# Kernel optimization log

Hardware: AMD Instinct MI355X
Metric: run time of the kernel (lower is better)

The kernel has to match this reference:

```python
import jax, jax.numpy as jnp
import numpy as np

B, S, HID, H = 4, 2048, 768, 12
HD = HID // H  # head dim = 64
EPS = 1e-12


def _linear(x, w, b):
    # x: [B,S,HID], w: [HID,OUT] (already transposed to in x out), b: [OUT]
    return jnp.einsum('bsi,io->bso', x, w) + b


def _heads(x):
    # [B,S,HID] -> [B,H,S,HD]
    return x.reshape(B, S, H, HD).transpose(0, 2, 1, 3)


def _layernorm(x, g, b):
    mu = jnp.mean(x, axis=-1, keepdims=True)
    var = jnp.mean(jnp.square(x - mu), axis=-1, keepdims=True)
    return (x - mu) * jax.lax.rsqrt(var + EPS) * g + b


def _attend(q, k, v, mask):
    # q:[B,H,Sq,HD] k,v:[B,H,Sk,HD] mask:[B,1,1,Sk] additive
    scores = jnp.einsum('bhqd,bhkd->bhqk', q, k) / np.float32(np.sqrt(HD)) + mask
    probs = jax.nn.softmax(scores, axis=-1)  # dropout is identity in eval
    ctx = jnp.einsum('bhqk,bhkd->bhqd', probs, v)
    return ctx.transpose(0, 2, 1, 3).reshape(B, S, HID)


def setup_inputs() -> dict:
    key = jax.random.key(0)
    ks = jax.random.split(key, 20)
    std = 0.02
    mkw = lambda k: (jax.random.normal(k, (HID, HID), jnp.float32) * std)
    inp = {
        'input_tensor1': jax.random.normal(ks[0], (B, S, HID), jnp.float32),
        'attention_mask1': jnp.zeros((B, 1, 1, S), jnp.float32),
        'input_tensor2': jax.random.normal(ks[1], (B, S, HID), jnp.float32),
        'attention_mask2': jnp.zeros((B, 1, 1, S), jnp.float32),
        'q1_w': mkw(ks[2]), 'q1_b': jnp.zeros(HID),
        'k1_w': mkw(ks[3]), 'k1_b': jnp.zeros(HID),
        'v1_w': mkw(ks[4]), 'v1_b': jnp.zeros(HID),
        'q2_w': mkw(ks[5]), 'q2_b': jnp.zeros(HID),
        'k2_w': mkw(ks[6]), 'k2_b': jnp.zeros(HID),
        'v2_w': mkw(ks[7]), 'v2_b': jnp.zeros(HID),
        'd1_w': mkw(ks[8]), 'd1_b': jnp.zeros(HID),
        'd2_w': mkw(ks[9]), 'd2_b': jnp.zeros(HID),
        'ln1_g': jnp.ones(HID), 'ln1_b': jnp.zeros(HID),
        'ln2_g': jnp.ones(HID), 'ln2_b': jnp.zeros(HID),
    }
    return inp


def reference(input_tensor1, attention_mask1, input_tensor2, attention_mask2,
              q1_w, q1_b, k1_w, k1_b, v1_w, v1_b,
              q2_w, q2_b, k2_w, k2_b, v2_w, v2_b,
              d1_w, d1_b, d2_w, d2_b, ln1_g, ln1_b, ln2_g, ln2_b):
    q1 = _heads(_linear(input_tensor1, q1_w, q1_b))
    k1 = _heads(_linear(input_tensor1, k1_w, k1_b))
    v1 = _heads(_linear(input_tensor1, v1_w, v1_b))
    q2 = _heads(_linear(input_tensor2, q2_w, q2_b))
    k2 = _heads(_linear(input_tensor2, k2_w, k2_b))
    v2 = _heads(_linear(input_tensor2, v2_w, v2_b))
    # stream1 context: queries from stream2 attend keys/values of stream1
    ctx1 = _attend(q2, k1, v1, attention_mask1)
    # stream2 context: queries from stream1 attend keys/values of stream2
    ctx2 = _attend(q1, k2, v2, attention_mask2)
    h1 = _layernorm(_linear(ctx1, d1_w, d1_b) + input_tensor1, ln1_g, ln1_b)
    h2 = _layernorm(_linear(ctx2, d2_w, d2_b) + input_tensor2, ln2_g, ln2_b)
    return (h1, h2)
```

## Files before the change

### kernel.cpp

```cpp
#include <hip/hip_runtime.h>
#include <hip/hip_bf16.h>

#define BB   4
#define SS   2048
#define HID_ 768
#define NH   12
#define HD_  64
#define MR   8192
#define XELEMS 6291456

typedef __attribute__((ext_vector_type(8))) short short8;
typedef __attribute__((ext_vector_type(4))) float floatx4;

__device__ __forceinline__ unsigned short f2bf(float f) {
  union { float f; unsigned int u; } x; x.f = f;
  unsigned int r = x.u + 0x7fffu + ((x.u >> 16) & 1u);
  return (unsigned short)(r >> 16);
}

__device__ __forceinline__ unsigned int cvt_pk_bf16(float lo, float hi) {
  unsigned int r;
  asm("v_cvt_pk_bf16_f32 %0, %1, %2" : "=v"(r) : "v"(lo), "v"(hi));
  return r;
}

__device__ __forceinline__ void gload_lds16(const unsigned short* g, unsigned short* l) {
  __builtin_amdgcn_global_load_lds(
      (const __attribute__((address_space(1))) unsigned int*)g,
      (__attribute__((address_space(3))) unsigned int*)l, 16, 0, 0);
}

struct CastArgs { const float* src[2]; unsigned short* dst[2]; };

__global__ __launch_bounds__(256)
void cast_kernel(CastArgs a) {
  const int z = blockIdx.y;
  int i = (blockIdx.x * 256 + threadIdx.x) * 4;
  float4 v = *(const float4*)(a.src[z] + i);
  ushort4 o;
  o.x = f2bf(v.x); o.y = f2bf(v.y); o.z = f2bf(v.z); o.w = f2bf(v.w);
  *(ushort4*)(a.dst[z] + i) = o;
}

struct WArgs { const float* src[8]; unsigned short* dst[8]; };

__global__ __launch_bounds__(256)
void wcast_kernel(WArgs args) {
  __shared__ float tile[32][33];
  const int w = blockIdx.z;
  const float* __restrict__ src = args.src[w];
  unsigned short* __restrict__ dst = args.dst[w];
  const int n0 = blockIdx.x * 32, k0 = blockIdx.y * 32;
  const int tx = threadIdx.x & 31, ty = threadIdx.x >> 5;
  #pragma unroll
  for (int i = 0; i < 4; ++i)
    tile[ty + 8 * i][tx] = src[(size_t)(k0 + ty + 8 * i) * HID_ + n0 + tx];
  __syncthreads();
  #pragma unroll
  for (int i = 0; i < 4; ++i)
    dst[(size_t)(n0 + ty + 8 * i) * HID_ + k0 + tx] = f2bf(tile[tx][ty + 8 * i]);
}

struct GemmArgs {
  const unsigned short* A[6];
  const unsigned short* Bt[6];
  const float* bias[6];
  const float* resid[6];
  unsigned short* outb[6];
  float* outf[6];
  int tmode[6];
};

template <int MODE>
__global__ __launch_bounds__(256)
void gemm_kernel(GemmArgs args) {
  const int z = blockIdx.z;
  const unsigned short* __restrict__ A  = args.A[z];
  const unsigned short* __restrict__ Bt = args.Bt[z];
  const int m0 = blockIdx.x * 128;
  const int n0 = blockIdx.y * 128;

  __shared__ __align__(16) unsigned short a_sh[128 * 32];
  __shared__ __align__(16) unsigned short b_sh[128 * 32];

  const int tid  = threadIdx.x;
  const int lane = tid & 63;
  const int wave = tid >> 6;
  const int wm = (wave & 1) * 64;
  const int wn = (wave >> 1) * 64;
  const int l15 = lane & 15;
  const int ko  = lane >> 4;

  floatx4 acc[4][4];
  #pragma unroll
  for (int mt = 0; mt < 4; ++mt)
    #pragma unroll
    for (int nt = 0; nt < 4; ++nt) {
      floatx4 zz = {0.f, 0.f, 0.f, 0.f};
      acc[mt][nt] = zz;
    }

  const int ch0 = wave * 2;
  size_t aoff[2], boff[2];
  unsigned short *adst[2], *bdst[2];
  #pragma unroll
  for (int j = 0; j < 2; ++j) {
    const int ch = ch0 + j;
    const int row = ch * 16 + (lane >> 2);
    const int col = (lane & 3) * 8;
    aoff[j] = (size_t)(m0 + row) * 768 + col;
    boff[j] = (size_t)(n0 + row) * 768 + col;
    adst[j] = a_sh + ch * 512 + lane * 8;
    bdst[j] = b_sh + ch * 512 + lane * 8;
  }

  for (int k0 = 0; k0 < 768; k0 += 32) {
    #pragma unroll
    for (int j = 0; j < 2; ++j) {
      gload_lds16(A  + aoff[j] + k0, adst[j]);
      gload_lds16(Bt + boff[j] + k0, bdst[j]);
    }
    __syncthreads();
    short8 af[4], bfr[4];
    #pragma unroll
    for (int t = 0; t < 4; ++t) {
      af[t]  = *(const short8*)(a_sh + (wm + t * 16 + l15) * 32 + ko * 8);
      bfr[t] = *(const short8*)(b_sh + (wn + t * 16 + l15) * 32 + ko * 8);
    }
    #pragma unroll
    for (int mt = 0; mt < 4; ++mt)
      #pragma unroll
      for (int nt = 0; nt < 4; ++nt)
        acc[mt][nt] = __builtin_amdgcn_mfma_f32_16x16x32_bf16(af[mt], bfr[nt], acc[mt][nt], 0, 0, 0);
    __syncthreads();
  }

  if (MODE == 0) {
    const float* __restrict__ bias = args.bias[z];
    unsigned short* __restrict__ out = args.outb[z];
    if (args.tmode[z] == 0) {
      #pragma unroll
      for (int mt = 0; mt < 4; ++mt) {
        const int gm = m0 + wm + mt * 16 + ko * 4;
        #pragma unroll
        for (int nt = 0; nt < 4; ++nt) {
          const int gn = n0 + wn + nt * 16 + l15;
          const float bv = bias[gn];
          #pragma unroll
          for (int r = 0; r < 4; ++r)
            out[(size_t)(gm + r) * 768 + gn] = f2bf(acc[mt][nt][r] + bv);
        }
      }
    } else {
      #pragma unroll
      for (int mt = 0; mt < 4; ++mt) {
        const int gm = m0 + wm + mt * 16 + ko * 4;
        const int bb_ = gm >> 11;
        const int s   = gm & 2047;
        #pragma unroll
        for (int nt = 0; nt < 4; ++nt) {
          const int gn = n0 + wn + nt * 16 + l15;
          const float bv = bias[gn];
          const int h = gn >> 6, d = gn & 63;
          ushort4 o4;
          o4.x = f2bf(acc[mt][nt][0] + bv);
          o4.y = f2bf(acc[mt][nt][1] + bv);
          o4.z = f2bf(acc[mt][nt][2] + bv);
          o4.w = f2bf(acc[mt][nt][3] + bv);
          *(ushort4*)(out + ((size_t)((bb_ * 12 + h) * 64 + d)) * 2048 + s) = o4;
        }
      }
    }
  } else {
    const float* __restrict__ bias  = args.bias[z];
    const float* __restrict__ resid = args.resid[z];
    float* __restrict__ out = args.outf[z];
    #pragma unroll
    for (int mt = 0; mt < 4; ++mt) {
      const int gm = m0 + wm + mt * 16 + ko * 4;
      #pragma unroll
      for (int nt = 0; nt < 4; ++nt) {
        const int gn = n0 + wn + nt * 16 + l15;
        const float bv = bias[gn];
        #pragma unroll
        for (int r = 0; r < 4; ++r)
          out[(size_t)(gm + r) * 768 + gn] = acc[mt][nt][r] + bv + resid[(size_t)(gm + r) * 768 + gn];
      }
    }
  }
}

struct AttnArgs {
  const unsigned short* q[2];
  const unsigned short* k[2];
  const unsigned short* vt[2];
  const float* mask[2];
  unsigned short* ctx[2];
};

__global__ __launch_bounds__(256, 2)
void attn_kernel(AttnArgs args) {
  const int z = blockIdx.z;
  const int b = z >> 1, w = z & 1;
  const int h = blockIdx.y;
  const int q0 = blockIdx.x * 256;

  const unsigned short* __restrict__ Q  = args.q[1 - w];
  const unsigned short* __restrict__ K  = args.k[w];
  const unsigned short* __restrict__ Vt = args.vt[w] + ((size_t)(b * 12 + h)) * 64 * 2048;
  const float* __restrict__ mask = args.mask[w] + (size_t)b * SS;
  unsigned short* __restrict__ O = args.ctx[w];

  __shared__ __align__(16) unsigned short kv_sh[2][8192];
  __shared__ __align__(16) unsigned short p_sh[4][64 * 40];

  const int tid  = threadIdx.x;
  const int lane = tid & 63;
  const int wave = tid >> 6;
  const int l15 = lane & 15;
  const int lq  = lane >> 4;
  const int sw8 = (lq ^ (l15 & 3)) * 8;

  const unsigned short* gbase;
  int gadv;
  int goff[4];
  {
    const int rl = lane >> 2;
    const int jb = (lane & 3) ^ (rl & 3);
    if (wave < 2) {
      gbase = K + (size_t)(b * SS) * 768 + h * 64 + (wave & 1) * 32;
      gadv  = 64 * 768;
      #pragma unroll
      for (int j = 0; j < 4; ++j) goff[j] = (j * 16 + rl) * 768 + jb * 8;
    } else {
      gbase = Vt + (wave & 1) * 32;
      gadv  = 64;
      #pragma unroll
      for (int j = 0; j < 4; ++j) goff[j] = (j * 16 + rl) * 2048 + jb * 8;
    }
  }

  short8 qf[4][2];
  #pragma unroll
  for (int mt = 0; mt < 4; ++mt) {
    const size_t qrow = (size_t)(b * SS + q0 + wave * 64 + mt * 16 + l15) * 768 + h * 64;
    qf[mt][0] = *(const short8*)(Q + qrow + lq * 8);
    qf[mt][1] = *(const short8*)(Q + qrow + 32 + lq * 8);
  }

  floatx4 oacc[4][4];
  #pragma unroll
  for (int mt = 0; mt < 4; ++mt)
    #pragma unroll
    for (int nt = 0; nt < 4; ++nt) { floatx4 zz = {0.f,0.f,0.f,0.f}; oacc[mt][nt] = zz; }
  float lad[4];
  #pragma unroll
  for (int mt = 0; mt < 4; ++mt) lad[mt] = 0.f;

  const float SCL2 = 0.125f * 1.4426950408889634f;
  const float L2E  = 1.4426950408889634f;

  float4 mk_cur[4], mk_nxt[4];
  #pragma unroll
  for (int nt = 0; nt < 4; ++nt) mk_cur[nt] = *(const float4*)(mask + nt * 16 + lq * 4);
  #pragma unroll
  for (int j = 0; j < 4; ++j)
    gload_lds16(gbase + goff[j], &kv_sh[0][0] + (wave * 4 + j) * 512);
  gbase += gadv;

  unsigned short* const pw = p_sh[wave];
  const int NT = SS / 64;

  for (int t = 0; t < NT; ++t) {
    const int cb = t & 1;
    if (t + 1 < NT) {
      const int kt1 = (t + 1) * 64;
      #pragma unroll
      for (int nt = 0; nt < 4; ++nt)
        mk_nxt[nt] = *(const float4*)(mask + kt1 + nt * 16 + lq * 4);
      #pragma unroll
      for (int j = 0; j < 4; ++j)
        gload_lds16(gbase + goff[j], &kv_sh[cb ^ 1][0] + (wave * 4 + j) * 512);
      gbase += gadv;
      asm volatile("s_waitcnt vmcnt(8)" ::: "memory");
    } else {
      asm volatile("s_waitcnt vmcnt(0)" ::: "memory");
    }
    __builtin_amdgcn_s_barrier();
    asm volatile("" ::: "memory");

    const unsigned short* kb = &kv_sh[cb][0];
    const unsigned short* vb = &kv_sh[cb][4096];

    #pragma unroll
    for (int ksh = 0; ksh < 2; ++ksh) {
      #pragma unroll
      for (int ntk = 0; ntk < 2; ++ntk) {
        const int nt = ksh * 2 + ntk;
        const int ro = (nt * 16 + l15) * 32 + sw8;
        const short8 kf0 = *(const short8*)(kb + ro);
        const short8 kf1 = *(const short8*)(kb + 2048 + ro);
        const float m0 = mk_cur[nt].x * L2E;
        const float m1 = mk_cur[nt].y * L2E;
        const float m2 = mk_cur[nt].z * L2E;
        const float m3 = mk_cur[nt].w * L2E;
        #pragma unroll
        for (int mt = 0; mt < 4; ++mt) {
          floatx4 zz = {0.f,0.f,0.f,0.f};
          floatx4 sacc = __builtin_amdgcn_mfma_f32_16x16x32_bf16(kf0, qf[mt][0], zz, 0, 0, 0);
          sacc = __builtin_amdgcn_mfma_f32_16x16x32_bf16(kf1, qf[mt][1], sacc, 0, 0, 0);
          const float p0 = __builtin_amdgcn_exp2f(sacc[0] * SCL2 + m0);
          const float p1 = __builtin_amdgcn_exp2f(sacc[1] * SCL2 + m1);
          const float p2 = __builtin_amdgcn_exp2f(sacc[2] * SCL2 + m2);
          const float p3 = __builtin_amdgcn_exp2f(sacc[3] * SCL2 + m3);
          lad[mt] += (p0 + p1) + (p2 + p3);
          uint2 pk2;
          pk2.x = cvt_pk_bf16(p0, p1);
          pk2.y = cvt_pk_bf16(p2, p3);
          *(uint2*)(pw + (mt * 16 + l15) * 40 + ntk * 16 + lq * 4) = pk2;
        }
      }
      short8 vf[4];
      #pragma unroll
      for (int ntd = 0; ntd < 4; ++ntd)
        vf[ntd] = *(const short8*)(vb + ksh * 2048 + (ntd * 16 + l15) * 32 + sw8);
      #pragma unroll
      for (int mt = 0; mt < 4; ++mt) {
        const short8 pf = *(const short8*)(pw + (mt * 16 + l15) * 40 + lq * 8);
        #pragma unroll
        for (int ntd = 0; ntd < 4; ++ntd)
          oacc[mt][ntd] = __builtin_amdgcn_mfma_f32_16x16x32_bf16(pf, vf[ntd], oacc[mt][ntd], 0, 0, 0);
      }
    }

    asm volatile("" ::: "memory");
    __builtin_amdgcn_s_barrier();
    asm volatile("" ::: "memory");

    #pragma unroll
    for (int nt = 0; nt < 4; ++nt) mk_cur[nt] = mk_nxt[nt];
  }

  #pragma unroll
  for (int mt = 0; mt < 4; ++mt) {
    float ls = lad[mt];
    ls += __shfl_xor(ls, 16);
    ls += __shfl_xor(ls, 32);
    const float linv = 1.f / ls;
    float inv[4];
    #pragma unroll
    for (int r = 0; r < 4; ++r) inv[r] = __shfl(linv, lq * 4 + r, 16);
    #pragma unroll
    for (int nt = 0; nt < 4; ++nt) {
      #pragma unroll
      for (int r = 0; r < 4; ++r) {
        const int gq = q0 + wave * 64 + mt * 16 + lq * 4 + r;
        const int gd = h * 64 + nt * 16 + l15;
        O[(size_t)(b * SS + gq) * 768 + gd] = f2bf(oacc[mt][nt][r] * inv[r]);
      }
    }
  }
}

struct LnArgs { const float* src[2]; const float* g[2]; const float* bta[2]; float* out[2]; };

__global__ __launch_bounds__(256)
void ln_kernel(LnArgs a) {
  const int z = blockIdx.y;
  const int row = blockIdx.x;
  const int tid = threadIdx.x;
  const float* x = a.src[z] + (size_t)row * 768;
  const float* g = a.g[z];
  const float* bta = a.bta[z];
  const float v0 = x[tid], v1 = x[tid + 256], v2 = x[tid + 512];
  float sum = v0 + v1 + v2;
  float sq  = v0 * v0 + v1 * v1 + v2 * v2;
  #pragma unroll
  for (int d = 1; d < 64; d <<= 1) {
    sum += __shfl_xor(sum, d, 64);
    sq  += __shfl_xor(sq, d, 64);
  }
  __shared__ float ssum[4], ssq[4];
  const int wave = tid >> 6, lane = tid & 63;
  if (lane == 0) { ssum[wave] = sum; ssq[wave] = sq; }
  __syncthreads();
  sum = ssum[0] + ssum[1] + ssum[2] + ssum[3];
  sq  = ssq[0] + ssq[1] + ssq[2] + ssq[3];
  const float mean = sum * (1.f / 768.f);
  const float var  = sq * (1.f / 768.f) - mean * mean;
  const float rs   = rsqrtf(var + 1e-12f);
  float* o = a.out[z] + (size_t)row * 768;
  o[tid]       = (v0 - mean) * rs * g[tid]       + bta[tid];
  o[tid + 256] = (v1 - mean) * rs * g[tid + 256] + bta[tid + 256];
  o[tid + 512] = (v2 - mean) * rs * g[tid + 512] + bta[tid + 512];
}

extern "C" void kernel_launch(void* const* d_in, const int* in_sizes, int n_in,
                              void* d_out, int out_size, void* d_ws, size_t ws_size,
                              hipStream_t stream) {
  const float* x1    = (const float*)d_in[0];
  const float* mask1 = (const float*)d_in[1];
  const float* x2    = (const float*)d_in[2];
  const float* mask2 = (const float*)d_in[3];

  char* ws = (char*)d_ws;
  const size_t SZ_X = (size_t)MR * HID_ * 2;
  const size_t SZ_W = (size_t)HID_ * HID_ * 2;

  unsigned short* xb0 = (unsigned short*)(ws);
  unsigned short* xb1 = (unsigned short*)(ws + SZ_X);
  unsigned short* wtb[8];
  for (int i = 0; i < 8; ++i) wtb[i] = (unsigned short*)(ws + 2 * SZ_X + i * SZ_W);
  char* qbase = ws + 2 * SZ_X + 8 * SZ_W;
  unsigned short* qkvb[6];
  for (int i = 0; i < 6; ++i) qkvb[i] = (unsigned short*)(qbase + i * SZ_X);
  unsigned short* ctxb[2];
  ctxb[0] = (unsigned short*)(qbase + 6 * SZ_X);
  ctxb[1] = (unsigned short*)(qbase + 7 * SZ_X);
  float* projb[2];
  projb[0] = (float*)(qbase);
  projb[1] = (float*)(qbase + 2 * SZ_X);

  CastArgs ca;
  ca.src[0] = x1; ca.src[1] = x2; ca.dst[0] = xb0; ca.dst[1] = xb1;
  cast_kernel<<<dim3(XELEMS / 1024, 2), 256, 0, stream>>>(ca);

  WArgs wa;
  for (int z = 0; z < 8; ++z) { wa.src[z] = (const float*)d_in[4 + 2 * z]; wa.dst[z] = wtb[z]; }
  wcast_kernel<<<dim3(24, 24, 8), 256, 0, stream>>>(wa);

  GemmArgs ga = {};
  for (int z = 0; z < 6; ++z) {
    ga.A[z]    = (z < 3) ? xb0 : xb1;
    ga.Bt[z]   = wtb[z];
    ga.bias[z] = (const float*)d_in[5 + 2 * z];
    ga.outb[z] = qkvb[z];
    ga.tmode[z] = (z == 2 || z == 5) ? 2 : 0;
  }
  gemm_kernel<0><<<dim3(64, 6, 6), 256, 0, stream>>>(ga);

  AttnArgs aa;
  aa.q[0] = qkvb[0]; aa.q[1] = qkvb[3];
  aa.k[0] = qkvb[1]; aa.k[1] = qkvb[4];
  aa.vt[0] = qkvb[2]; aa.vt[1] = qkvb[5];
  aa.mask[0] = mask1; aa.mask[1] = mask2;
  aa.ctx[0] = ctxb[0]; aa.ctx[1] = ctxb[1];
  attn_kernel<<<dim3(8, 12, 8), 256, 0, stream>>>(aa);

  GemmArgs gp = {};
  for (int w = 0; w < 2; ++w) {
    gp.A[w]     = ctxb[w];
    gp.Bt[w]    = wtb[6 + w];
    gp.bias[w]  = (const float*)d_in[17 + 2 * w];
    gp.resid[w] = (w == 0) ? x1 : x2;
    gp.outf[w]  = projb[w];
  }
  gemm_kernel<1><<<dim3(64, 6, 2), 256, 0, stream>>>(gp);

  float* out = (float*)d_out;
  LnArgs la;
  la.src[0] = projb[0]; la.src[1] = projb[1];
  la.g[0] = (const float*)d_in[20]; la.bta[0] = (const float*)d_in[21];
  la.g[1] = (const float*)d_in[22]; la.bta[1] = (const float*)d_in[23];
  la.out[0] = out; la.out[1] = out + XELEMS;
  ln_kernel<<<dim3(MR, 2), 256, 0, stream>>>(la);
}
```

Measured before the change: 460.5 us.

## Keep softmax probabilities in registers and compute PV transposed with 16x16x16 MFMA

Removes the per-wave LDS round trip for the probability tile. Packed bf16 probabilities now feed 16x16x16 bf16 MFMAs directly, computing O transposed with V as the A operand, so the score-accumulator layout matches the B-operand layout. The mask is preloaded once into LDS with the log2e scaling applied, instead of being prefetched from global memory every tile. The epilogue writes packed bf16 pairs per row. The tradeoffs are twice as many smaller-K MFMA instructions, inline asm that hides them from compiler scheduling, and a hand-placed s_nop hazard guard.

```diff
diff --git a/kernel.cpp b/kernel.cpp
--- a/kernel.cpp
+++ b/kernel.cpp
@@ -11,6 +11,7 @@
 
 typedef __attribute__((ext_vector_type(8))) short short8;
 typedef __attribute__((ext_vector_type(4))) float floatx4;
+typedef __attribute__((ext_vector_type(2))) unsigned int uintx2;
 
 __device__ __forceinline__ unsigned short f2bf(float f) {
   union { float f; unsigned int u; } x; x.f = f;
@@ -212,7 +213,7 @@
   unsigned short* __restrict__ O = args.ctx[w];
 
   __shared__ __align__(16) unsigned short kv_sh[2][8192];
-  __shared__ __align__(16) unsigned short p_sh[4][64 * 40];
+  __shared__ __align__(16) float msk_sh[2048];
 
   const int tid  = threadIdx.x;
   const int lane = tid & 63;
@@ -220,6 +221,18 @@
   const int l15 = lane & 15;
   const int lq  = lane >> 4;
   const int sw8 = (lq ^ (l15 & 3)) * 8;
+
+  const float SCL2 = 0.125f * 1.4426950408889634f;
+  const float L2E  = 1.4426950408889634f;
+
+  {
+    float4 m0 = *(const float4*)(mask + tid * 8);
+    float4 m1 = *(const float4*)(mask + tid * 8 + 4);
+    m0.x *= L2E; m0.y *= L2E; m0.z *= L2E; m0.w *= L2E;
+    m1.x *= L2E; m1.y *= L2E; m1.z *= L2E; m1.w *= L2E;
+    *(float4*)(msk_sh + tid * 8)     = m0;
+    *(float4*)(msk_sh + tid * 8 + 4) = m1;
+  }
 
   const unsigned short* gbase;
   int gadv;
@@ -248,41 +261,32 @@
     qf[mt][1] = *(const short8*)(Q + qrow + 32 + lq * 8);
   }
 
-  floatx4 oacc[4][4];
+  floatx4 oaccT[4][4];
   #pragma unroll
   for (int mt = 0; mt < 4; ++mt)
     #pragma unroll
-    for (int nt = 0; nt < 4; ++nt) { floatx4 zz = {0.f,0.f,0.f,0.f}; oacc[mt][nt] = zz; }
+    for (int nt = 0; nt < 4; ++nt) { floatx4 zz = {0.f,0.f,0.f,0.f}; oaccT[mt][nt] = zz; }
   float lad[4];
   #pragma unroll
   for (int mt = 0; mt < 4; ++mt) lad[mt] = 0.f;
 
-  const float SCL2 = 0.125f * 1.4426950408889634f;
-  const float L2E  = 1.4426950408889634f;
-
-  float4 mk_cur[4], mk_nxt[4];
-  #pragma unroll
-  for (int nt = 0; nt < 4; ++nt) mk_cur[nt] = *(const float4*)(mask + nt * 16 + lq * 4);
+  asm volatile("s_waitcnt lgkmcnt(0)" ::: "memory");
+
   #pragma unroll
   for (int j = 0; j < 4; ++j)
     gload_lds16(gbase + goff[j], &kv_sh[0][0] + (wave * 4 + j) * 512);
   gbase += gadv;
 
-  unsigned short* const pw = p_sh[wave];
   const int NT = SS / 64;
 
   for (int t = 0; t < NT; ++t) {
     const int cb = t & 1;
     if (t + 1 < NT) {
-      const int kt1 = (t + 1) * 64;
-      #pragma unroll
-      for (int nt = 0; nt < 4; ++nt)
-        mk_nxt[nt] = *(const float4*)(mask + kt1 + nt * 16 + lq * 4);
       #pragma unroll
       for (int j = 0; j < 4; ++j)
         gload_lds16(gbase + goff[j], &kv_sh[cb ^ 1][0] + (wave * 4 + j) * 512);
       gbase += gadv;
-      asm volatile("s_waitcnt vmcnt(8)" ::: "memory");
+      asm volatile("s_waitcnt vmcnt(4)" ::: "memory");
     } else {
       asm volatile("s_waitcnt vmcnt(0)" ::: "memory");
     }
@@ -292,72 +296,76 @@
     const unsigned short* kb = &kv_sh[cb][0];
     const unsigned short* vb = &kv_sh[cb][4096];
 
+    float4 mk[4];
+    #pragma unroll
+    for (int nt = 0; nt < 4; ++nt)
+      mk[nt] = *(const float4*)(msk_sh + t * 64 + nt * 16 + lq * 4);
+
     #pragma unroll
     for (int ksh = 0; ksh < 2; ++ksh) {
+      uintx2 vf[2][4];
+      #pragma unroll
+      for (int ntk = 0; ntk < 2; ++ntk) {
+        const int blk = ((ntk * 2 + (lq >> 1)) ^ (l15 & 3)) * 8 + (lq & 1) * 4;
+        #pragma unroll
+        for (int ntd = 0; ntd < 4; ++ntd)
+          vf[ntk][ntd] = *(const uintx2*)(vb + ksh * 2048 + (ntd * 16 + l15) * 32 + blk);
+      }
+
+      uintx2 pk[4][2];
       #pragma unroll
       for (int ntk = 0; ntk < 2; ++ntk) {
         const int nt = ksh * 2 + ntk;
         const int ro = (nt * 16 + l15) * 32 + sw8;
         const short8 kf0 = *(const short8*)(kb + ro);
         const short8 kf1 = *(const short8*)(kb + 2048 + ro);
-        const float m0 = mk_cur[nt].x * L2E;
-        const float m1 = mk_cur[nt].y * L2E;
-        const float m2 = mk_cur[nt].z * L2E;
-        const float m3 = mk_cur[nt].w * L2E;
         #pragma unroll
         for (int mt = 0; mt < 4; ++mt) {
           floatx4 zz = {0.f,0.f,0.f,0.f};
           floatx4 sacc = __builtin_amdgcn_mfma_f32_16x16x32_bf16(kf0, qf[mt][0], zz, 0, 0, 0);
           sacc = __builtin_amdgcn_mfma_f32_16x16x32_bf16(kf1, qf[mt][1], sacc, 0, 0, 0);
-          const float p0 = __builtin_amdgcn_exp2f(sacc[0] * SCL2 + m0);
-          const float p1 = __builtin_amdgcn_exp2f(sacc[1] * SCL2 + m1);
-          const float p2 = __builtin_amdgcn_exp2f(sacc[2] * SCL2 + m2);
-          const float p3 = __builtin_amdgcn_exp2f(sacc[3] * SCL2 + m3);
+          const float p0 = __builtin_amdgcn_exp2f(sacc[0] * SCL2 + mk[nt].x);
+          const float p1 = __builtin_amdgcn_exp2f(sacc[1] * SCL2 + mk[nt].y);
+          const float p2 = __builtin_amdgcn_exp2f(sacc[2] * SCL2 + mk[nt].z);
+          const float p3 = __builtin_amdgcn_exp2f(sacc[3] * SCL2 + mk[nt].w);
           lad[mt] += (p0 + p1) + (p2 + p3);
-          uint2 pk2;
-          pk2.x = cvt_pk_bf16(p0, p1);
-          pk2.y = cvt_pk_bf16(p2, p3);
-          *(uint2*)(pw + (mt * 16 + l15) * 40 + ntk * 16 + lq * 4) = pk2;
+          pk[mt][ntk].x = cvt_pk_bf16(p0, p1);
+          pk[mt][ntk].y = cvt_pk_bf16(p2, p3);
         }
       }
-      short8 vf[4];
-      #pragma unroll
-      for (int ntd = 0; ntd < 4; ++ntd)
-        vf[ntd] = *(const short8*)(vb + ksh * 2048 + (ntd * 16 + l15) * 32 + sw8);
-      #pragma unroll
-      for (int mt = 0; mt < 4; ++mt) {
-        const short8 pf = *(const short8*)(pw + (mt * 16 + l15) * 40 + lq * 8);
-        #pragma unroll
-        for (int ntd = 0; ntd < 4; ++ntd)
-          oacc[mt][ntd] = __builtin_amdgcn_mfma_f32_16x16x32_bf16(pf, vf[ntd], oacc[mt][ntd], 0, 0, 0);
-      }
+
+      #pragma unroll
+      for (int mt = 0; mt < 4; ++mt)
+        #pragma unroll
+        for (int ntd = 0; ntd < 4; ++ntd) {
+          asm("v_mfma_f32_16x16x16_bf16 %0, %1, %2, %0"
+              : "+v"(oaccT[mt][ntd]) : "v"(vf[0][ntd]), "v"(pk[mt][0]));
+          asm("v_mfma_f32_16x16x16_bf16 %0, %1, %2, %0"
+              : "+v"(oaccT[mt][ntd]) : "v"(vf[1][ntd]), "v"(pk[mt][1]));
+        }
     }
 
     asm volatile("" ::: "memory");
     __builtin_amdgcn_s_barrier();
     asm volatile("" ::: "memory");
-
-    #pragma unroll
-    for (int nt = 0; nt < 4; ++nt) mk_cur[nt] = mk_nxt[nt];
-  }
+  }
+
+  asm volatile("s_nop 7\n\ts_nop 7" ::: "memory");
 
   #pragma unroll
   for (int mt = 0; mt < 4; ++mt) {
     float ls = lad[mt];
     ls += __shfl_xor(ls, 16);
     ls += __shfl_xor(ls, 32);
-    const float linv = 1.f / ls;
-    float inv[4];
-    #pragma unroll
-    for (int r = 0; r < 4; ++r) inv[r] = __shfl(linv, lq * 4 + r, 16);
-    #pragma unroll
-    for (int nt = 0; nt < 4; ++nt) {
-      #pragma unroll
-      for (int r = 0; r < 4; ++r) {
-        const int gq = q0 + wave * 64 + mt * 16 + lq * 4 + r;
-        const int gd = h * 64 + nt * 16 + l15;
-        O[(size_t)(b * SS + gq) * 768 + gd] = f2bf(oacc[mt][nt][r] * inv[r]);
-      }
+    const float inv = 1.f / ls;
+    const int gq = q0 + wave * 64 + mt * 16 + l15;
+    unsigned short* orow = O + (size_t)(b * SS + gq) * 768 + h * 64 + lq * 4;
+    #pragma unroll
+    for (int ntd = 0; ntd < 4; ++ntd) {
+      uintx2 o2;
+      o2.x = cvt_pk_bf16(oaccT[mt][ntd][0] * inv, oaccT[mt][ntd][1] * inv);
+      o2.y = cvt_pk_bf16(oaccT[mt][ntd][2] * inv, oaccT[mt][ntd][3] * inv);
+      *(uintx2*)(orow + ntd * 16) = o2;
     }
   }
 }
```

After: 467.8 us. Within noise of the previous version (+1.6%).
